# Kernel tuning notes

Measured on AMD Instinct MI355X. Metric: run time of the kernel, lower is better.

## Reference

```python
import jax, jax.numpy as jnp
import numpy as np

B, C, H, W = 64, 512, 8, 8
K = 100            # num_class
H1, HID, L = 64, 128, 32   # ae_hidden[0], fixed hidd, ae_latent
CLIP = 100.0       # CSSRClassifier.clip_len
RED = -0.1         # model='pcssr' -> -1, times gamma=0.1
PUSH_THRESH = 10000.0


def setup_inputs() -> dict:
    key = jax.random.key(0)
    ks = jax.random.split(key, 9)
    s = lambda fan_in: 1.0 / np.sqrt(fan_in)  # kaiming-ish 1x1 conv init scale
    return {
        "x": jax.random.normal(ks[0], (B, C, H, W), jnp.float32),
        "ycls": jax.random.randint(ks[1], (B,), 0, K),
        "safe_margin_all": jax.random.normal(ks[2], (K,), jnp.float32),
        "safe_distance_all": jax.random.normal(ks[3], (K,), jnp.float32),
        "W1": jax.random.normal(ks[4], (K, H1, C), jnp.float32) * s(C),
        "W2": jax.random.normal(ks[5], (K, HID, H1), jnp.float32) * s(H1),
        "W3": jax.random.normal(ks[6], (K, L, HID), jnp.float32) * s(HID),
        "prototypes": jax.random.normal(ks[7], (K, L, H, W), jnp.float32),
        "prototypes1": jax.random.normal(ks[8], (K, L, H, W), jnp.float32),
    }


def reference(x, ycls, safe_margin_all, safe_distance_all, W1, W2, W3, prototypes, prototypes1):
    P = H * W
    xf = x.reshape(B, C, P)
    # per-class 1x1-conv encoder (tanh after every conv), batched over classes k
    h = jnp.tanh(jnp.einsum('koc,bcp->kbop', W1, xf))      # [K,B,H1,P]
    h = jnp.tanh(jnp.einsum('koi,kbip->kbop', W2, h))      # [K,B,HID,P]
    lt = jnp.tanh(jnp.einsum('koi,kbip->kbop', W3, h))     # [K,B,L,P]
    p = prototypes.reshape(K, 1, L, P)
    p1 = prototypes1.reshape(K, 1, L, P)
    # squared-L2 distance over channel dim, scaled by reduction, clipped
    er = jnp.clip(jnp.sum((lt - p) ** 2, axis=2) * RED, -CLIP, CLIP)    # [K,B,P]
    er1 = jnp.clip(jnp.sum((lt - p1) ** 2, axis=2) * RED, -CLIP, CLIP)  # [K,B,P]
    # training losses (pull on er1, push on er), vectorized across classes
    f = jnp.sum(er, axis=2)    # [K,B] spatial-summed errors
    f1 = jnp.sum(er1, axis=2)  # [K,B]
    cls_ids = jnp.arange(K)[:, None]
    mask_eq = (ycls[None, :] == cls_ids).astype(f.dtype)   # [K,B]
    n_eq = jnp.sum(mask_eq, axis=1)
    pull = jnp.sum(jnp.where(n_eq > 0,
                             jnp.sum(f1 * mask_eq, axis=1) / jnp.maximum(n_eq, 1.0),
                             0.0))
    comb = (1.0 - mask_eq) * (f < PUSH_THRESH).astype(f.dtype)
    n_comb = jnp.sum(comb, axis=1)
    push = jnp.sum(jnp.where(n_comb > 0,
                             jnp.sum(f * comb, axis=1) / jnp.maximum(n_comb, 1.0),
                             0.0))
    # cat per-class [B,1,H,W] errors along dim 1 -> [B,K,H,W]
    logits = jnp.transpose(er, (1, 0, 2)).reshape(B, K, H, W)
    logits1 = jnp.transpose(er1, (1, 0, 2)).reshape(B, K, H, W)
    return logits, logits1, pull, push
```

## Files before the change

### kernel.cpp

```cpp
#include <hip/hip_runtime.h>

typedef short  s16x8  __attribute__((ext_vector_type(8)));
typedef float  f32x16 __attribute__((ext_vector_type(16)));
typedef unsigned short u16;
typedef unsigned int   u32;
typedef unsigned long long u64b;

#define MFMA32(a,b,c) __builtin_amdgcn_mfma_f32_32x32x16_bf16((a),(b),(c),0,0,0)
#define KCLS 100
#define VMCNT(n) asm volatile("s_waitcnt vmcnt(" #n ")" ::: "memory")
#define BAR()    __builtin_amdgcn_s_barrier()
#define SCHEDB() __builtin_amdgcn_sched_barrier(0)

__device__ __forceinline__ u16 f2bf(float f) {
  return (u16)(__builtin_bit_cast(unsigned, f) >> 16);
}

__device__ __forceinline__ u32 pk2bf(float lo, float hi) {
  return (__builtin_bit_cast(u32, lo) >> 16) | (__builtin_bit_cast(u32, hi) & 0xffff0000u);
}

__device__ __forceinline__ float tanh_fast(float x) {
  float e = __builtin_amdgcn_exp2f(x * 2.8853900817779268f);
  return 1.0f - 2.0f * __builtin_amdgcn_rcpf(e + 1.0f);
}

__device__ __forceinline__ void ld_lds16(const void* g, void* l) {
  __builtin_amdgcn_global_load_lds(
      (const __attribute__((address_space(1))) unsigned char*)g,
      (__attribute__((address_space(3))) unsigned char*)l, 16, 0, 0);
}

__global__ void prep(const float* __restrict__ x, const float* __restrict__ w1,
                     const float* __restrict__ w2, const float* __restrict__ w3,
                     u16* __restrict__ xF, u16* __restrict__ W1F,
                     u16* __restrict__ W2F, u16* __restrict__ W3F,
                     float* __restrict__ fz, float* __restrict__ out2) {
  __shared__ float tile[64][65];
  const int bid = blockIdx.x, t = threadIdx.x;
  if (bid == 0 && t < 2) out2[t] = 0.f;
  if (bid < 512) {
    const int b = bid >> 3, ck = bid & 7;
    #pragma unroll
    for (int j = 0; j < 4; j++) {
      int e4 = j * 1024 + t * 4;
      int c = e4 >> 6, p0 = e4 & 63;
      float4 v = *(const float4*)(x + ((size_t)b * 512 + ck * 64 + c) * 64 + p0);
      tile[c][p0] = v.x; tile[c][p0 + 1] = v.y; tile[c][p0 + 2] = v.z; tile[c][p0 + 3] = v.w;
    }
    __syncthreads();
    #pragma unroll
    for (int i = 0; i < 2; i++) {
      int s = i * 256 + t;
      int ksl = s >> 7, ph = (s >> 6) & 1, lane = s & 63;
      int cb = ksl * 16 + (lane >> 5) * 8, pp = ph * 32 + (lane & 31);
      u16 o[8];
      #pragma unroll
      for (int jj = 0; jj < 8; jj++) o[jj] = f2bf(tile[cb + jj][pp]);
      *(uint4*)(xF + (((size_t)b * 64 + (ck * 4 + ksl) * 2 + ph) * 512) + lane * 8) = *(uint4*)o;
    }
  } else if (bid < 1312) {
    int base = (bid - 512) * 512;
    #pragma unroll
    for (int i = 0; i < 2; i++) {
      int s = base + i * 256 + t;
      int frag = s >> 6, lane = s & 63;
      int k = frag >> 6, fr = frag & 63;
      int m = (fr & 1) * 32 + (lane & 31);
      int c0 = (fr >> 1) * 16 + (lane >> 5) * 8;
      const float* src = w1 + ((size_t)k * 64 + m) * 512 + c0;
      float4 a = *(const float4*)src, b4 = *(const float4*)(src + 4);
      u16 o[8] = { f2bf(a.x), f2bf(a.y), f2bf(a.z), f2bf(a.w),
                   f2bf(b4.x), f2bf(b4.y), f2bf(b4.z), f2bf(b4.w) };
      *(uint4*)(W1F + ((size_t)frag * 512) + lane * 8) = *(uint4*)o;
    }
  } else if (bid < 1512) {
    int base = (bid - 1312) * 512;
    #pragma unroll
    for (int i = 0; i < 2; i++) {
      int s = base + i * 256 + t;
      int frag = s >> 6, lane = s & 63;
      int k = frag >> 4, fr = frag & 15;
      int m = (fr & 3) * 32 + (lane & 31);
      int c0 = (fr >> 2) * 16 + (lane >> 5) * 8;
      const float* src = w2 + ((size_t)k * 128 + m) * 64 + c0;
      float4 a = *(const float4*)src, b4 = *(const float4*)(src + 4);
      u16 o[8] = { f2bf(a.x), f2bf(a.y), f2bf(a.z), f2bf(a.w),
                   f2bf(b4.x), f2bf(b4.y), f2bf(b4.z), f2bf(b4.w) };
      *(uint4*)(W2F + ((size_t)frag * 512) + lane * 8) = *(uint4*)o;
    }
  } else if (bid < 1612) {
    int base = (bid - 1512) * 512;
    #pragma unroll
    for (int i = 0; i < 2; i++) {
      int s = base + i * 256 + t;
      int frag = s >> 6, lane = s & 63;
      int k = frag >> 3, kb = frag & 7;
      int m = lane & 31;
      int c0 = kb * 16 + (lane >> 5) * 8;
      const float* src = w3 + ((size_t)k * 32 + m) * 128 + c0;
      float4 a = *(const float4*)src, b4 = *(const float4*)(src + 4);
      u16 o[8] = { f2bf(a.x), f2bf(a.y), f2bf(a.z), f2bf(a.w),
                   f2bf(b4.x), f2bf(b4.y), f2bf(b4.z), f2bf(b4.w) };
      *(uint4*)(W3F + ((size_t)frag * 512) + lane * 8) = *(uint4*)o;
    }
  } else {
    int i4 = (bid - 1612) * 256 + t;
    if (i4 < 3200) {
      float4 z = {0.f, 0.f, 0.f, 0.f};
      *(float4*)(fz + (size_t)i4 * 4) = z;
    }
  }
}

template<int GG>
__device__ __forceinline__ s16x8 mk_bfrag(const f32x16 a) {
  u32 P0 = pk2bf(tanh_fast(a[8 * GG + 0]), tanh_fast(a[8 * GG + 1]));
  u32 P1 = pk2bf(tanh_fast(a[8 * GG + 2]), tanh_fast(a[8 * GG + 3]));
  u32 Q0 = pk2bf(tanh_fast(a[8 * GG + 4]), tanh_fast(a[8 * GG + 5]));
  u32 Q1 = pk2bf(tanh_fast(a[8 * GG + 6]), tanh_fast(a[8 * GG + 7]));
  asm("v_permlane32_swap_b32 %0, %1" : "+v"(P0), "+v"(Q0));
  asm("v_permlane32_swap_b32 %0, %1" : "+v"(P1), "+v"(Q1));
  int4 wv = { (int)P0, (int)P1, (int)Q0, (int)Q1 };
  return __builtin_bit_cast(s16x8, wv);
}

__global__ __launch_bounds__(256, 3) void cssr_main(
    const u16* __restrict__ W1F, const u16* __restrict__ W2F, const u16* __restrict__ W3F,
    const u16* __restrict__ xF, const float* __restrict__ protos,
    const float* __restrict__ protos1, float* __restrict__ out,
    float* __restrict__ fw, float* __restrict__ f1w)
{
  __shared__ u16 pool[2][12288];
  const int bid = blockIdx.x;
  const int k = bid >> 5, bpair = bid & 31;
  const int tid = threadIdx.x, w = tid >> 6, lane = tid & 63;
  const int bq = w >> 1, ph = w & 1;
  const int b = bpair * 2 + bq;
  const int h = lane >> 5, nn = lane & 31;

  const u16* sp[6];
  int dfo[6];
  #pragma unroll
  for (int i = 0; i < 6; i++) {
    int f = w * 6 + i;
    dfo[i] = f * 512;
    if (f < 8) {
      int ksl = f >> 1, mt = f & 1;
      sp[i] = W1F + ((size_t)k * 64 + ksl * 2 + mt) * 512 + lane * 8;
    } else {
      int g = f - 8, wv = g >> 2, ksl = g & 3;
      int bs = bpair * 2 + (wv >> 1), ps = wv & 1;
      sp[i] = xF + ((size_t)bs * 64 + ksl * 2 + ps) * 512 + lane * 8;
    }
  }

  #pragma unroll
  for (int i = 0; i < 6; i++) { ld_lds16(sp[i], &pool[0][dfo[i]]); sp[i] += 4096; }
  VMCNT(0); BAR();

  f32x16 acc1[2] = {};
  #pragma unroll
  for (int ci = 0; ci < 8; ci++) {
    const int cb = ci & 1;
    if (ci < 7) {
      #pragma unroll
      for (int i = 0; i < 6; i++) { ld_lds16(sp[i], &pool[cb ^ 1][dfo[i]]); sp[i] += 4096; }
      VMCNT(6);
    } else {
      #pragma unroll
      for (int j = 0; j < 4; j++) {
        int f = w * 4 + j;
        ld_lds16(W2F + ((size_t)k * 16 + f) * 512 + lane * 8, &pool[0][f * 512]);
      }
      VMCNT(4);
    }
    BAR(); SCHEDB();
    const u16* bu = pool[cb];
    #pragma unroll
    for (int ksl = 0; ksl < 4; ksl++) {
      s16x8 A0 = *(const s16x8*)(bu + (ksl * 2 + 0) * 512 + lane * 8);
      s16x8 A1 = *(const s16x8*)(bu + (ksl * 2 + 1) * 512 + lane * 8);
      s16x8 B  = *(const s16x8*)(bu + (8 + w * 4 + ksl) * 512 + lane * 8);
      acc1[0] = MFMA32(A0, B, acc1[0]);
      acc1[1] = MFMA32(A1, B, acc1[1]);
    }
    BAR();
  }

  #pragma unroll
  for (int j = 0; j < 2; j++) {
    int f = w * 2 + j;
    ld_lds16(W3F + ((size_t)k * 8 + f) * 512 + lane * 8, &pool[1][f * 512]);
  }

  s16x8 b1[4];
  b1[0] = mk_bfrag<0>(acc1[0]); b1[1] = mk_bfrag<1>(acc1[0]);
  b1[2] = mk_bfrag<0>(acc1[1]); b1[3] = mk_bfrag<1>(acc1[1]);

  VMCNT(2); BAR(); SCHEDB();

  f32x16 acc2[4] = {};
  #pragma unroll
  for (int kb = 0; kb < 4; kb++) {
    #pragma unroll
    for (int m4 = 0; m4 < 4; m4++) {
      s16x8 A = *(const s16x8*)(&pool[0][(kb * 4 + m4) * 512] + lane * 8);
      acc2[m4] = MFMA32(A, b1[kb], acc2[m4]);
    }
  }

  s16x8 b2[8];
  b2[0] = mk_bfrag<0>(acc2[0]); b2[1] = mk_bfrag<1>(acc2[0]);
  b2[2] = mk_bfrag<0>(acc2[1]); b2[3] = mk_bfrag<1>(acc2[1]);
  b2[4] = mk_bfrag<0>(acc2[2]); b2[5] = mk_bfrag<1>(acc2[2]);
  b2[6] = mk_bfrag<0>(acc2[3]); b2[7] = mk_bfrag<1>(acc2[3]);

  VMCNT(0); BAR(); SCHEDB();

  const int p = ph * 32 + nn;
  const float* pr  = protos  + (size_t)k * 2048 + p;
  const float* pr1 = protos1 + (size_t)k * 2048 + p;
  float prv[16], pr1v[16];
  #pragma unroll
  for (int g = 0; g < 4; g++) {
    #pragma unroll
    for (int q = 0; q < 4; q++) {
      int m = q + 8 * g + 4 * h;
      prv [g * 4 + q] = pr [m * 64];
      pr1v[g * 4 + q] = pr1[m * 64];
    }
  }

  f32x16 acc3 = {};
  #pragma unroll
  for (int kb = 0; kb < 8; kb++) {
    s16x8 A = *(const s16x8*)(&pool[1][kb * 512] + lane * 8);
    acc3 = MFMA32(A, b2[kb], acc3);
  }

  float d2 = 0.f, d21 = 0.f;
  #pragma unroll
  for (int g = 0; g < 4; g++) {
    #pragma unroll
    for (int q = 0; q < 4; q++) {
      float lt = tanh_fast(acc3[g * 4 + q]);
      float d = lt - prv [g * 4 + q];  d2  += d * d;
      float e = lt - pr1v[g * 4 + q];  d21 += e * e;
    }
  }
  d2 += __shfl_xor(d2, 32); d21 += __shfl_xor(d21, 32);
  float er  = fminf(fmaxf(d2  * -0.1f, -100.f), 100.f);
  float er1 = fminf(fmaxf(d21 * -0.1f, -100.f), 100.f);
  if (h == 0) {
    out[(size_t)b * 6400 + k * 64 + p]          = er;
    out[409600 + (size_t)b * 6400 + k * 64 + p] = er1;
  }
  float s = er, s1 = er1;
  s += __shfl_xor(s, 1);  s1 += __shfl_xor(s1, 1);
  s += __shfl_xor(s, 2);  s1 += __shfl_xor(s1, 2);
  s += __shfl_xor(s, 4);  s1 += __shfl_xor(s1, 4);
  s += __shfl_xor(s, 8);  s1 += __shfl_xor(s1, 8);
  s += __shfl_xor(s, 16); s1 += __shfl_xor(s1, 16);
  if (lane == 0) {
    atomicAdd(&fw [k * 64 + b], s);
    atomicAdd(&f1w[k * 64 + b], s1);
  }
}

__global__ void finalize(const float* __restrict__ f, const float* __restrict__ f1,
                         const int* __restrict__ ycls, float* __restrict__ out2) {
  const int k = blockIdx.x, b = threadIdx.x;
  float fv = f[k * 64 + b], f1v = f1[k * 64 + b];
  bool eq = (ycls[b] == k);
  bool cb = (!eq) && (fv < 10000.f);
  float s1 = eq ? f1v : 0.f, ne = eq ? 1.f : 0.f;
  float s  = cb ? fv  : 0.f, nc = cb ? 1.f : 0.f;
  #pragma unroll
  for (int o = 1; o < 64; o <<= 1) {
    s1 += __shfl_xor(s1, o); ne += __shfl_xor(ne, o);
    s  += __shfl_xor(s,  o); nc += __shfl_xor(nc, o);
  }
  if (b == 0) {
    if (ne > 0.f) atomicAdd(&out2[0], s1 / ne);
    if (nc > 0.f) atomicAdd(&out2[1], s / nc);
  }
}

extern "C" void kernel_launch(void* const* d_in, const int* in_sizes, int n_in,
                              void* d_out, int out_size, void* d_ws, size_t ws_size,
                              hipStream_t stream) {
  const float* x     = (const float*)d_in[0];
  const int*   ycls  = (const int*)d_in[1];
  const float* W1    = (const float*)d_in[4];
  const float* W2    = (const float*)d_in[5];
  const float* W3    = (const float*)d_in[6];
  const float* prot  = (const float*)d_in[7];
  const float* prot1 = (const float*)d_in[8];
  float* out = (float*)d_out;

  char* ws = (char*)d_ws;
  u16*  xFb = (u16*)(ws);
  u16*  W1F = (u16*)(ws + 4194304);
  u16*  W2F = (u16*)(ws + 10747904);
  u16*  W3F = (u16*)(ws + 12386304);
  float* fw  = (float*)(ws + 13205504);
  float* f1w = (float*)(ws + 13231104);

  prep<<<1625, 256, 0, stream>>>(x, W1, W2, W3, xFb, W1F, W2F, W3F,
                                 fw, out + 819200);
  cssr_main<<<KCLS * 32, 256, 0, stream>>>(W1F, W2F, W3F, xFb, prot, prot1,
                                           out, fw, f1w);
  finalize<<<KCLS, 64, 0, stream>>>(fw, f1w, ycls, out + 819200);
}
```

Measured before the change: 144.9 us.

## Load x B-fragments directly to registers, shrink LDS, raise occupancy

The x operand for the first layer now goes straight from global memory into registers with a one-stage register prefetch. Only the W1 tiles are staged through LDS, and the W2/W3 tiles get their own disjoint regions issued early, so the LDS footprint drops from 48KB to 40KB and launch bounds rise to 4 blocks per CU. The change also adds s_setprio around the MFMA loops, uses v_perm for the bf16 packing, and drops the sched_barriers. The intent is less LDS traffic, fewer barriers and better latency hiding from higher occupancy, at the cost of more register pressure.

```diff
diff --git a/kernel.cpp b/kernel.cpp
--- a/kernel.cpp
+++ b/kernel.cpp
@@ -10,14 +10,18 @@
 #define KCLS 100
 #define VMCNT(n) asm volatile("s_waitcnt vmcnt(" #n ")" ::: "memory")
 #define BAR()    __builtin_amdgcn_s_barrier()
-#define SCHEDB() __builtin_amdgcn_sched_barrier(0)
 
 __device__ __forceinline__ u16 f2bf(float f) {
   return (u16)(__builtin_bit_cast(unsigned, f) >> 16);
 }
 
 __device__ __forceinline__ u32 pk2bf(float lo, float hi) {
+#if __has_builtin(__builtin_amdgcn_perm)
+  return __builtin_amdgcn_perm(__builtin_bit_cast(u32, hi),
+                               __builtin_bit_cast(u32, lo), 0x07060302u);
+#else
   return (__builtin_bit_cast(u32, lo) >> 16) | (__builtin_bit_cast(u32, hi) & 0xffff0000u);
+#endif
 }
 
 __device__ __forceinline__ float tanh_fast(float x) {
@@ -125,13 +129,13 @@
   return __builtin_bit_cast(s16x8, wv);
 }
 
-__global__ __launch_bounds__(256, 3) void cssr_main(
+__global__ __launch_bounds__(256, 4) void cssr_main(
     const u16* __restrict__ W1F, const u16* __restrict__ W2F, const u16* __restrict__ W3F,
     const u16* __restrict__ xF, const float* __restrict__ protos,
     const float* __restrict__ protos1, float* __restrict__ out,
     float* __restrict__ fw, float* __restrict__ f1w)
 {
-  __shared__ u16 pool[2][12288];
+  __shared__ u16 pool[20480];
   const int bid = blockIdx.x;
   const int k = bid >> 5, bpair = bid & 31;
   const int tid = threadIdx.x, w = tid >> 6, lane = tid & 63;
@@ -139,25 +143,15 @@
   const int b = bpair * 2 + bq;
   const int h = lane >> 5, nn = lane & 31;
 
-  const u16* sp[6];
-  int dfo[6];
-  #pragma unroll
-  for (int i = 0; i < 6; i++) {
-    int f = w * 6 + i;
-    dfo[i] = f * 512;
-    if (f < 8) {
-      int ksl = f >> 1, mt = f & 1;
-      sp[i] = W1F + ((size_t)k * 64 + ksl * 2 + mt) * 512 + lane * 8;
-    } else {
-      int g = f - 8, wv = g >> 2, ksl = g & 3;
-      int bs = bpair * 2 + (wv >> 1), ps = wv & 1;
-      sp[i] = xF + ((size_t)bs * 64 + ksl * 2 + ps) * 512 + lane * 8;
-    }
-  }
-
-  #pragma unroll
-  for (int i = 0; i < 6; i++) { ld_lds16(sp[i], &pool[0][dfo[i]]); sp[i] += 4096; }
-  VMCNT(0); BAR();
+  const u16* xw  = xF  + ((size_t)b * 64) * 512 + lane * 8;
+  const u16* w1w = W1F + ((size_t)k * 64) * 512 + lane * 8;
+
+  s16x8 Bc[4], Bn[4];
+  #pragma unroll
+  for (int ksl = 0; ksl < 4; ksl++)
+    Bc[ksl] = *(const s16x8*)(xw + (ksl * 2 + ph) * 512);
+  ld_lds16(w1w + (w * 2 + 0) * 512, &pool[(2 * w + 0) * 512]);
+  ld_lds16(w1w + (w * 2 + 1) * 512, &pool[(2 * w + 1) * 512]);
 
   f32x16 acc1[2] = {};
   #pragma unroll
@@ -165,48 +159,66 @@
     const int cb = ci & 1;
     if (ci < 7) {
       #pragma unroll
-      for (int i = 0; i < 6; i++) { ld_lds16(sp[i], &pool[cb ^ 1][dfo[i]]); sp[i] += 4096; }
-      VMCNT(6);
+      for (int ksl = 0; ksl < 4; ksl++)
+        Bn[ksl] = *(const s16x8*)(xw + (((ci + 1) * 4 + ksl) * 2 + ph) * 512);
+      ld_lds16(w1w + (((ci + 1) * 4 + w) * 2 + 0) * 512, &pool[(cb ^ 1) * 4096 + (2 * w + 0) * 512]);
+      ld_lds16(w1w + (((ci + 1) * 4 + w) * 2 + 1) * 512, &pool[(cb ^ 1) * 4096 + (2 * w + 1) * 512]);
     } else {
       #pragma unroll
-      for (int j = 0; j < 4; j++) {
-        int f = w * 4 + j;
-        ld_lds16(W2F + ((size_t)k * 16 + f) * 512 + lane * 8, &pool[0][f * 512]);
-      }
-      VMCNT(4);
-    }
-    BAR(); SCHEDB();
-    const u16* bu = pool[cb];
+      for (int j = 0; j < 4; j++)
+        ld_lds16(W2F + ((size_t)k * 16 + w * 4 + j) * 512 + lane * 8,
+                 &pool[8192 + (w * 4 + j) * 512]);
+      ld_lds16(W3F + ((size_t)k * 8 + w * 2 + 0) * 512 + lane * 8, &pool[16384 + (w * 2 + 0) * 512]);
+      ld_lds16(W3F + ((size_t)k * 8 + w * 2 + 1) * 512 + lane * 8, &pool[16384 + (w * 2 + 1) * 512]);
+    }
+    VMCNT(6); BAR();
+    __builtin_amdgcn_s_setprio(1);
     #pragma unroll
     for (int ksl = 0; ksl < 4; ksl++) {
-      s16x8 A0 = *(const s16x8*)(bu + (ksl * 2 + 0) * 512 + lane * 8);
-      s16x8 A1 = *(const s16x8*)(bu + (ksl * 2 + 1) * 512 + lane * 8);
-      s16x8 B  = *(const s16x8*)(bu + (8 + w * 4 + ksl) * 512 + lane * 8);
-      acc1[0] = MFMA32(A0, B, acc1[0]);
-      acc1[1] = MFMA32(A1, B, acc1[1]);
-    }
-    BAR();
-  }
-
-  #pragma unroll
-  for (int j = 0; j < 2; j++) {
-    int f = w * 2 + j;
-    ld_lds16(W3F + ((size_t)k * 8 + f) * 512 + lane * 8, &pool[1][f * 512]);
+      s16x8 A0 = *(const s16x8*)&pool[cb * 4096 + (ksl * 2 + 0) * 512 + lane * 8];
+      s16x8 A1 = *(const s16x8*)&pool[cb * 4096 + (ksl * 2 + 1) * 512 + lane * 8];
+      acc1[0] = MFMA32(A0, Bc[ksl], acc1[0]);
+      acc1[1] = MFMA32(A1, Bc[ksl], acc1[1]);
+    }
+    __builtin_amdgcn_s_setprio(0);
+    if (ci < 7) {
+      #pragma unroll
+      for (int ksl = 0; ksl < 4; ksl++) Bc[ksl] = Bn[ksl];
+      BAR();
+    }
   }
 
   s16x8 b1[4];
   b1[0] = mk_bfrag<0>(acc1[0]); b1[1] = mk_bfrag<1>(acc1[0]);
   b1[2] = mk_bfrag<0>(acc1[1]); b1[3] = mk_bfrag<1>(acc1[1]);
 
-  VMCNT(2); BAR(); SCHEDB();
+  VMCNT(2); BAR();
 
   f32x16 acc2[4] = {};
+  __builtin_amdgcn_s_setprio(1);
   #pragma unroll
   for (int kb = 0; kb < 4; kb++) {
     #pragma unroll
     for (int m4 = 0; m4 < 4; m4++) {
-      s16x8 A = *(const s16x8*)(&pool[0][(kb * 4 + m4) * 512] + lane * 8);
+      s16x8 A = *(const s16x8*)&pool[8192 + (kb * 4 + m4) * 512 + lane * 8];
       acc2[m4] = MFMA32(A, b1[kb], acc2[m4]);
+    }
+  }
+  __builtin_amdgcn_s_setprio(0);
+
+  VMCNT(0); BAR();
+
+  const int p = ph * 32 + nn;
+  const float* pr  = protos  + (size_t)k * 2048 + p;
+  const float* pr1 = protos1 + (size_t)k * 2048 + p;
+  float prv[16], pr1v[16];
+  #pragma unroll
+  for (int g = 0; g < 4; g++) {
+    #pragma unroll
+    for (int q = 0; q < 4; q++) {
+      int m = q + 8 * g + 4 * h;
+      prv [g * 4 + q] = pr [m * 64];
+      pr1v[g * 4 + q] = pr1[m * 64];
     }
   }
 
@@ -216,28 +228,14 @@
   b2[4] = mk_bfrag<0>(acc2[2]); b2[5] = mk_bfrag<1>(acc2[2]);
   b2[6] = mk_bfrag<0>(acc2[3]); b2[7] = mk_bfrag<1>(acc2[3]);
 
-  VMCNT(0); BAR(); SCHEDB();
-
-  const int p = ph * 32 + nn;
-  const float* pr  = protos  + (size_t)k * 2048 + p;
-  const float* pr1 = protos1 + (size_t)k * 2048 + p;
-  float prv[16], pr1v[16];
-  #pragma unroll
-  for (int g = 0; g < 4; g++) {
-    #pragma unroll
-    for (int q = 0; q < 4; q++) {
-      int m = q + 8 * g + 4 * h;
-      prv [g * 4 + q] = pr [m * 64];
-      pr1v[g * 4 + q] = pr1[m * 64];
-    }
-  }
-
   f32x16 acc3 = {};
+  __builtin_amdgcn_s_setprio(1);
   #pragma unroll
   for (int kb = 0; kb < 8; kb++) {
-    s16x8 A = *(const s16x8*)(&pool[1][kb * 512] + lane * 8);
+    s16x8 A = *(const s16x8*)&pool[16384 + kb * 512 + lane * 8];
     acc3 = MFMA32(A, b2[kb], acc3);
   }
+  __builtin_amdgcn_s_setprio(0);
 
   float d2 = 0.f, d21 = 0.f;
   #pragma unroll
```

Result: faster. 142.0 us (-2.0%).
